# Optimization experiments

Measured on AMD Instinct MI355X. Metric: run time of the kernel, lower is better.

Reference implementation:

```python
import jax, jax.numpy as jnp
import numpy as np
import math

K = 30   # neighbors
T = 9    # num_kernel

def sparsemax(z):
    # sparsemax along last axis
    zs = jnp.sort(z, axis=-1)[..., ::-1]
    rng = jnp.arange(1, z.shape[-1] + 1, dtype=z.dtype)
    cs = jnp.cumsum(zs, axis=-1)
    support = (1.0 + rng * zs) > cs
    kz = jnp.sum(support, axis=-1, keepdims=True)
    tau = (jnp.take_along_axis(cs, kz - 1, axis=-1) - 1.0) / kz.astype(z.dtype)
    return jnp.maximum(z - tau, 0.0)

def bn(x, g, b, axes, eps=1e-5):
    # batch-norm (training-mode batch stats), channel axis = 1
    m = jnp.mean(x, axes, keepdims=True)
    v = jnp.var(x, axes, keepdims=True)
    sh = [1] * x.ndim; sh[1] = -1
    return (x - m) / jnp.sqrt(v + eps) * g.reshape(sh) + b.reshape(sh)

def _forward(x, B_ff, mlp_W, permx, W1, b1, S1, W2, b2, S2, W3, b3, S3, W4, b4, S4,
             W5, g5, be5, L1, g6, be6, L2, bL2, g7, be7, L3, bL3):
    Bsz, _, N = x.shape
    pts = jnp.transpose(x, (0, 2, 1))                      # [B,N,3]
    # knn (DGCNN-style): negative squared distance, top-k (self first)
    xx = jnp.sum(pts * pts, -1)                            # [B,N]
    inner = jnp.einsum('bnc,bmc->bnm', pts, pts)
    negd = 2.0 * inner - xx[:, :, None] - xx[:, None, :]
    _, idx = jax.lax.top_k(negd, K)                        # [B,N,K] int32
    gather = jax.vmap(lambda f, i: f[i])                   # [B,N,F],[B,N,K]->[B,N,K,F]
    # Fourier features -> sparsemax basis weights -> per-point permatrix
    ng = gather(pts, idx)                                  # [B,N,K,3]
    xrep = jnp.broadcast_to(ng[:, :, :1, :], ng.shape)     # self repeated
    rel = ng - xrep
    sq = jnp.sum(rel * rel, -1, keepdims=True)
    dist = jnp.where(sq > 0, jnp.sqrt(jnp.where(sq > 0, sq, 1.0)), 0.0)  # safe norm
    feats = jnp.concatenate([xrep, rel, dist], -1).reshape(Bsz, N, 7 * K)
    ff = (2.0 * math.pi) * (feats @ B_ff)                  # [B,N,32]
    ff = jnp.concatenate([jnp.sin(ff), jnp.cos(ff)], -1)   # [B,N,64]
    w = sparsemax(ff @ mlp_W)                              # [B,N,16]
    P = jnp.einsum('bni,ikt->bnkt', w, permx)              # [B,N,K,T]

    def paiconv(f, W, b, S):  # f: [B,Cin,N]
        ft = jnp.transpose(f, (0, 2, 1))                   # [B,N,Cin]
        nb = gather(ft, idx)                               # [B,N,K,Cin]
        agg = jnp.einsum('bnkc,bnkt->bntc', nb, P).reshape(Bsz, N, -1)
        out = agg @ W + b + ft @ S                         # [B,N,Cout]
        return jnp.transpose(out, (0, 2, 1))

    gelu = lambda a: jax.nn.gelu(a, approximate=False)
    x1 = gelu(paiconv(x,  W1, b1, S1))
    x2 = gelu(paiconv(x1, W2, b2, S2))
    x3 = gelu(paiconv(x2, W3, b3, S3))
    x4 = gelu(paiconv(x3, W4, b4, S4))
    f = jnp.concatenate([x1, x2, x3, x4], 1)               # [B,512,N]
    f = jnp.einsum('bcn,ce->ben', f, W5)                   # conv5 (1x1)
    f = gelu(bn(f, g5, be5, (0, 2)))
    h = jnp.concatenate([jnp.max(f, -1), jnp.mean(f, -1)], -1)  # [B,2048]
    h = gelu(bn(h @ L1, g6, be6, (0,)))
    h = gelu(bn(h @ L2 + bL2, g7, be7, (0,)))
    return h @ L3 + bL3


def setup_inputs() -> dict:
    key = jax.random.key(0)
    ks = jax.random.split(key, 20)
    rn = lambda k_, sh, s=1.0: jax.random.normal(k_, sh, dtype=jnp.float32) * s
    B, N = 16, 1024
    inp = {}
    inp['x'] = rn(ks[0], (B, 3, N))
    inp['B_ff'] = rn(ks[1], (7 * K, 32))
    inp['mlp_W'] = rn(ks[2], (64, 16), 0.125)
    inp['permx'] = rn(ks[3], (16, K, T), 0.1)
    dims = [(3, 64), (64, 64), (64, 128), (128, 256)]
    for i, (ci, co) in enumerate(dims, 1):
        inp['W%d' % i] = rn(ks[3 + i], (T * ci, co), 1.0 / float(np.sqrt(T * ci)))
        inp['b%d' % i] = jnp.zeros((co,), jnp.float32)
        inp['S%d' % i] = rn(ks[7 + i], (ci, co), 1.0 / float(np.sqrt(ci)))
    inp['W5'] = rn(ks[12], (512, 1024), 1.0 / float(np.sqrt(512)))
    inp['g5'] = jnp.ones((1024,), jnp.float32); inp['be5'] = jnp.zeros((1024,), jnp.float32)
    inp['L1'] = rn(ks[13], (2048, 512), 1.0 / float(np.sqrt(2048)))
    inp['g6'] = jnp.ones((512,), jnp.float32); inp['be6'] = jnp.zeros((512,), jnp.float32)
    inp['L2'] = rn(ks[14], (512, 256), 1.0 / float(np.sqrt(512))); inp['bL2'] = jnp.zeros((256,), jnp.float32)
    inp['g7'] = jnp.ones((256,), jnp.float32); inp['be7'] = jnp.zeros((256,), jnp.float32)
    inp['L3'] = rn(ks[15], (256, 40), 1.0 / float(np.sqrt(256))); inp['bL3'] = jnp.zeros((40,), jnp.float32)
    return inp


def reference(x, B_ff, mlp_W, permx, W1, b1, S1, W2, b2, S2, W3, b3, S3, W4, b4, S4,
              W5, g5, be5, L1, g6, be6, L2, bL2, g7, be7, L3, bL3):
    return _forward(x, B_ff, mlp_W, permx, W1, b1, S1, W2, b2, S2, W3, b3, S3, W4, b4, S4,
                    W5, g5, be5, L1, g6, be6, L2, bL2, g7, be7, L3, bL3)
```

## Files before the change

kernel.cpp:

```cpp
#include <hip/hip_runtime.h>
#include <hip/hip_bf16.h>
#include <cstddef>

#define BSZ 16
#define NPT 1024
#define KNN 30
#define TKR 9
#define FLT_BIG 3.402823466e+38f

typedef unsigned short u16;
typedef __attribute__((ext_vector_type(8))) u16 u16x8;
typedef __attribute__((ext_vector_type(4))) float f32x4;

__device__ __forceinline__ float gelu_f(float x) {
    return 0.5f * x * (1.0f + erff(x * 0.7071067811865476f));
}

__device__ __forceinline__ u16 bf16_rne(float a) {
    unsigned u = __float_as_uint(a);
    u += 0x7FFFu + ((u >> 16) & 1u);
    return (u16)(u >> 16);
}
__device__ __forceinline__ float bf16_tof(u16 h) {
    return __uint_as_float(((unsigned)h) << 16);
}
__device__ __forceinline__ void split_bf16(float a, u16& h, u16& l) {
    h = bf16_rne(a);
    float r = a - bf16_tof(h);
    l = bf16_rne(r);
}

__device__ __forceinline__ size_t pack_off(int row, int k, int npanels_row) {
    return (size_t)((k >> 5) * npanels_row + (row >> 7)) * 4096
         + (size_t)(((k >> 3) & 3) * 1024 + (row & 127) * 8 + (k & 7));
}

__global__ __launch_bounds__(256) void prep_all(
    const float* __restrict__ x, float* __restrict__ pts,
    const float* __restrict__ W1, const float* __restrict__ S1, float* __restrict__ wz1,
    const float* __restrict__ W2, const float* __restrict__ S2, float* __restrict__ wz2,
    const float* __restrict__ W3, const float* __restrict__ S3, float* __restrict__ wz3,
    const float* __restrict__ W4, const float* __restrict__ S4,
    u16* __restrict__ w4tH, u16* __restrict__ w4tL) {
    int layer = blockIdx.y;
    int t = blockIdx.x * 256 + threadIdx.x;
    if (layer == 0) {
        if (t >= BSZ * NPT) return;
        int b = t >> 10, n = t & 1023;
        const float* xp = x + (size_t)b * 3 * NPT;
        pts[t * 3 + 0] = xp[n];
        pts[t * 3 + 1] = xp[NPT + n];
        pts[t * 3 + 2] = xp[2 * NPT + n];
        return;
    }
    if (layer == 4) {
        if (t >= 1280 * 256) return;
        int k = t >> 8, n = t & 255;
        float v = (k < 1152) ? W4[(size_t)k * 256 + n] : S4[(size_t)(k - 1152) * 256 + n];
        u16 h, l;
        split_bf16(v, h, l);
        size_t off = pack_off(n, k, 2);
        w4tH[off] = h;
        w4tL[off] = l;
        return;
    }
    const float *W, *S; float* WZ; int KW, KS, N, kpad;
    if (layer == 1)      { W = W1; S = S1; WZ = wz1; KW = 27;   KS = 3;   N = 64;  kpad = 32;  }
    else if (layer == 2) { W = W2; S = S2; WZ = wz2; KW = 576;  KS = 64;  N = 64;  kpad = 640; }
    else                 { W = W3; S = S3; WZ = wz3; KW = 576;  KS = 64;  N = 128; kpad = 640; }
    if (t >= kpad * N) return;
    int k = t / N, n = t - k * N;
    float v = 0.0f;
    if (k < KW) v = W[(size_t)k * N + n];
    else if (k < KW + KS) v = S[(size_t)(k - KW) * N + n];
    WZ[t] = v;
}

__global__ __launch_bounds__(256) void knn_basis_kernel(
    const float* __restrict__ pts, const float* __restrict__ B_ff,
    const float* __restrict__ mlp_W, const float* __restrict__ permx,
    int* __restrict__ idx, float* __restrict__ P) {
    __shared__ float npt[4][KNN * 3];
    __shared__ float feats[4][7 * KNN];
    __shared__ float sc[4][64];
    __shared__ float zl[4][16];
    __shared__ float w[4][16];
    __shared__ float sZs[4][16];
    __shared__ float sCs[4][16];
    __shared__ int sIds[4][KNN];
    int tid = threadIdx.x;
    int wave = tid >> 6, lane = tid & 63;
    int bn_ = blockIdx.x * 4 + wave;
    int b = bn_ >> 10;

    {
        double px = (double)pts[(size_t)bn_ * 3 + 0];
        double py = (double)pts[(size_t)bn_ * 3 + 1];
        double pz = (double)pts[(size_t)bn_ * 3 + 2];
        double xn = px * px + py * py + pz * pz;
        const float* pb = pts + (size_t)(b << 10) * 3;
        int base = lane * 16;
        unsigned mono[16];
        #pragma unroll
        for (int j = 0; j < 16; j++) {
            int m = base + j;
            double qx = (double)pb[m * 3 + 0];
            double qy = (double)pb[m * 3 + 1];
            double qz = (double)pb[m * 3 + 2];
            double inner = px * qx + py * qy + pz * qz;
            double xm = qx * qx + qy * qy + qz * qz;
            double cd = 2.0 * inner - xn - xm;
            float cf = (float)cd;
            unsigned bb = __float_as_uint(cf);
            mono[j] = (bb & 0x80000000u) ? ~bb : (bb | 0x80000000u);
        }
        unsigned alive = 0xFFFFu;
        unsigned c1v = 0u, c2v = 0u;
        int c1j = 0, c2j = 0;
        #pragma unroll
        for (int j = 0; j < 16; j++) {
            unsigned v = mono[j];
            if (v > c1v) { c2v = c1v; c2j = c1j; c1v = v; c1j = j; }
            else if (v > c2v) { c2v = v; c2j = j; }
        }
        bool have2 = true;
        for (int it = 0; it < KNN; it++) {
            unsigned m = c1v;
            #pragma unroll
            for (int s = 1; s < 64; s <<= 1) {
                unsigned ov = (unsigned)__shfl_xor((int)m, s, 64);
                m = (ov > m) ? ov : m;
            }
            unsigned long long ball = __ballot(c1v == m);
            int wlan = (int)__builtin_ctzll(ball);
            int jw = __shfl(c1j, wlan, 64);
            int bi = (wlan << 4) + jw;
            if (lane == it) sIds[wave][it] = bi;
            if (lane == wlan) {
                alive &= ~(1u << c1j);
                if (have2) {
                    c1v = c2v; c1j = c2j; have2 = false;
                } else {
                    unsigned a1 = 0u, a2 = 0u;
                    int j1 = 0, j2 = 0;
                    #pragma unroll
                    for (int j = 0; j < 16; j++) {
                        unsigned v = ((alive >> j) & 1u) ? mono[j] : 0u;
                        if (v > a1) { a2 = a1; j2 = j1; a1 = v; j1 = j; }
                        else if (v > a2) { a2 = v; j2 = j; }
                    }
                    c1v = a1; c1j = j1; c2v = a2; c2j = j2;
                    have2 = true;
                }
            }
        }
        __builtin_amdgcn_wave_barrier();
        if (lane < KNN) idx[(size_t)bn_ * KNN + lane] = sIds[wave][lane];
    }
    __syncthreads();

    if (lane < KNN) {
        int m = sIds[wave][lane];
        const float* q = pts + ((size_t)(b << 10) + m) * 3;
        npt[wave][lane * 3 + 0] = q[0];
        npt[wave][lane * 3 + 1] = q[1];
        npt[wave][lane * 3 + 2] = q[2];
    }
    __syncthreads();
    if (lane < KNN) {
        float sx = npt[wave][0], sy = npt[wave][1], sz = npt[wave][2];
        float rx = npt[wave][lane * 3 + 0] - sx;
        float ry = npt[wave][lane * 3 + 1] - sy;
        float rz = npt[wave][lane * 3 + 2] - sz;
        float sq = rx * rx + ry * ry + rz * rz;
        float dist = (sq > 0.0f) ? sqrtf(sq) : 0.0f;
        feats[wave][lane * 7 + 0] = sx;
        feats[wave][lane * 7 + 1] = sy;
        feats[wave][lane * 7 + 2] = sz;
        feats[wave][lane * 7 + 3] = rx;
        feats[wave][lane * 7 + 4] = ry;
        feats[wave][lane * 7 + 5] = rz;
        feats[wave][lane * 7 + 6] = dist;
    }
    __syncthreads();
    {
        int j = lane & 31;
        int half = lane >> 5;
        int i0 = half * 105;
        float acc = 0.0f;
        for (int i = i0; i < i0 + 105; i++) acc += feats[wave][i] * B_ff[i * 32 + j];
        acc += __shfl_xor(acc, 32, 64);
        if (half == 0) {
            float ffv = 6.283185307179586f * acc;
            sc[wave][j] = sinf(ffv);
            sc[wave][j + 32] = cosf(ffv);
        }
    }
    __syncthreads();
    {
        int j = lane & 15;
        int h = lane >> 4;
        float acc = 0.0f;
        for (int i = 16 * h; i < 16 * h + 16; i++) acc += sc[wave][i] * mlp_W[i * 16 + j];
        acc += __shfl_xor(acc, 16, 64);
        acc += __shfl_xor(acc, 32, 64);
        if (h == 0) zl[wave][j] = acc;
    }
    __syncthreads();
    {
        int l = lane & 15;
        float zv = zl[wave][l];
        int rank = 0;
        #pragma unroll
        for (int j = 0; j < 16; j++) {
            float zj = zl[wave][j];
            rank += (zj > zv || (zj == zv && j < l)) ? 1 : 0;
        }
        if (lane < 16) sZs[wave][rank] = zv;
        __builtin_amdgcn_wave_barrier();
        float cs = 0.0f;
        #pragma unroll
        for (int p = 0; p < 16; p++) {
            float zp = sZs[wave][p];
            cs += (p <= l) ? zp : 0.0f;
        }
        float zsl = sZs[wave][l];
        bool flag = (lane < 16) && (1.0f + (float)(l + 1) * zsl > cs);
        unsigned long long ball = __ballot(flag);
        int cnt = (int)__popcll(ball & 0xFFFFull);
        if (lane < 16) sCs[wave][l] = cs;
        __builtin_amdgcn_wave_barrier();
        float tau = (sCs[wave][cnt - 1] - 1.0f) / (float)cnt;
        if (lane < 16) w[wave][l] = fmaxf(zv - tau, 0.0f);
    }
    __syncthreads();
    float* Pp = P + (size_t)bn_ * (KNN * TKR);
    for (int e = lane; e < KNN * TKR; e += 64) {
        int k = e / TKR, t = e - TKR * k;
        float acc = 0.0f;
        for (int i = 0; i < 16; i++) acc += w[wave][i] * permx[(i * KNN + k) * TKR + t];
        Pp[e] = acc;
    }
}

template <int CIN>
__global__ __launch_bounds__(256) void agg_kernel(
    const float* __restrict__ ft, int ftst,
    const float* __restrict__ P, const int* __restrict__ idx,
    float* __restrict__ Z, int kpad) {
    __shared__ float sP[KNN * TKR];
    __shared__ float sNb[KNN * CIN];
    __shared__ int sIdx[KNN];
    int bn_ = blockIdx.x;
    int b = bn_ >> 10;
    int tid = threadIdx.x;
    if (tid < KNN) sIdx[tid] = idx[(size_t)bn_ * KNN + tid];
    for (int e = tid; e < KNN * TKR; e += 256) sP[e] = P[(size_t)bn_ * (KNN * TKR) + e];
    __syncthreads();
    for (int e = tid; e < KNN * CIN; e += 256) {
        int k = e / CIN, c = e - k * CIN;
        sNb[e] = ft[((size_t)(b << 10) + sIdx[k]) * ftst + c];
    }
    __syncthreads();
    float* zp = Z + (size_t)bn_ * kpad;
    const int KW = TKR * CIN;
    for (int e = tid; e < kpad; e += 256) {
        float v;
        if (e < KW) {
            int t = e / CIN, c = e - t * CIN;
            float acc = 0.0f;
            #pragma unroll
            for (int k = 0; k < KNN; k++) acc += sNb[k * CIN + c] * sP[k * TKR + t];
            v = acc;
        } else if (e < KW + CIN) {
            v = ft[(size_t)bn_ * ftst + (e - KW)];
        } else {
            v = 0.0f;
        }
        zp[e] = v;
    }
}

template <int CIN>
__global__ __launch_bounds__(256) void agg_v_kernel(
    const float* __restrict__ ft, int ftst,
    const float* __restrict__ P, const int* __restrict__ idx,
    float* __restrict__ Z, int kpad) {
    __shared__ float sP[KNN * TKR];
    __shared__ float sNb[KNN * CIN];
    __shared__ int sIdx[KNN];
    constexpr int C4 = CIN / 4;
    int bn_ = blockIdx.x;
    int b = bn_ >> 10;
    int tid = threadIdx.x;
    if (tid < KNN) sIdx[tid] = idx[(size_t)bn_ * KNN + tid];
    for (int e = tid; e < KNN * TKR; e += 256) sP[e] = P[(size_t)bn_ * (KNN * TKR) + e];
    __syncthreads();
    for (int e = tid; e < KNN * C4; e += 256) {
        int k = e / C4, c4 = (e - k * C4) * 4;
        *(float4*)&sNb[k * CIN + c4] =
            *(const float4*)&ft[((size_t)(b << 10) + sIdx[k]) * ftst + c4];
    }
    __syncthreads();
    float* zp = Z + (size_t)bn_ * kpad;
    const int KW = TKR * CIN;
    for (int e = tid; e < (kpad >> 2); e += 256) {
        int c0 = e * 4;
        float4 v;
        if (c0 < KW) {
            int t = c0 / CIN, c4 = c0 - t * CIN;
            float4 a = make_float4(0.f, 0.f, 0.f, 0.f);
            #pragma unroll
            for (int k = 0; k < KNN; k++) {
                float p = sP[k * TKR + t];
                float4 nb = *(const float4*)&sNb[k * CIN + c4];
                a.x += nb.x * p; a.y += nb.y * p;
                a.z += nb.z * p; a.w += nb.w * p;
            }
            v = a;
        } else if (c0 < KW + CIN) {
            v = *(const float4*)&ft[(size_t)bn_ * ftst + (c0 - KW)];
        } else {
            v = make_float4(0.f, 0.f, 0.f, 0.f);
        }
        *(float4*)&zp[c0] = v;
    }
}

__global__ __launch_bounds__(256) void agg_v_split4_kernel(
    const float* __restrict__ ft, int ftst,
    const float* __restrict__ P, const int* __restrict__ idx,
    u16* __restrict__ ZH, u16* __restrict__ ZL) {
    __shared__ int   sIdx4[4][KNN];
    __shared__ float sP4[4][KNN * TKR + 2];
    __shared__ float sNb4[4][KNN * 128];
    __shared__ __align__(16) u16 oH[4][640];
    __shared__ __align__(16) u16 oL[4][640];
    int tid = threadIdx.x;
    int wave = tid >> 6, lane = tid & 63;
    int r0 = blockIdx.x << 2;
    int b = r0 >> 10;
    const int KW = TKR * 128;

    if (tid < 4 * KNN) {
        int row = tid / KNN, k = tid - row * KNN;
        sIdx4[row][k] = idx[(size_t)(r0 + row) * KNN + k];
    }
    for (int e = tid; e < 4 * KNN * TKR; e += 256) {
        int row = e / (KNN * TKR), i = e - row * (KNN * TKR);
        sP4[row][i] = P[(size_t)(r0 + row) * (KNN * TKR) + i];
    }
    __syncthreads();
    for (int e = tid; e < 4 * KNN * 32; e += 256) {
        int row = e / (KNN * 32), rem = e - row * (KNN * 32);
        int k = rem >> 5, c4 = (rem & 31) << 2;
        *(float4*)&sNb4[row][k * 128 + c4] =
            *(const float4*)&ft[((size_t)(b << 10) + sIdx4[row][k]) * ftst + c4];
    }
    __syncthreads();

    #pragma unroll
    for (int pass = 0; pass < 2; pass++) {
        int ebase = pass * 640;
        for (int q = lane; q < 160; q += 64) {
            int e0 = ebase + q * 4;
            float4 v;
            if (e0 < KW) {
                int t = e0 >> 7, c = e0 & 127;
                float4 a = make_float4(0.f, 0.f, 0.f, 0.f);
                #pragma unroll
                for (int k = 0; k < KNN; k++) {
                    float p = sP4[wave][k * TKR + t];
                    float4 nb = *(const float4*)&sNb4[wave][k * 128 + c];
                    a.x += nb.x * p; a.y += nb.y * p;
                    a.z += nb.z * p; a.w += nb.w * p;
                }
                v = a;
            } else if (e0 < KW + 128) {
                v = *(const float4*)&ft[(size_t)(r0 + wave) * ftst + (e0 - KW)];
            } else {
                v = make_float4(0.f, 0.f, 0.f, 0.f);
            }
            u16 h[4], l[4];
            split_bf16(v.x, h[0], l[0]);
            split_bf16(v.y, h[1], l[1]);
            split_bf16(v.z, h[2], l[2]);
            split_bf16(v.w, h[3], l[3]);
            uint2 hv, lv;
            hv.x = (unsigned)h[0] | ((unsigned)h[1] << 16);
            hv.y = (unsigned)h[2] | ((unsigned)h[3] << 16);
            lv.x = (unsigned)l[0] | ((unsigned)l[1] << 16);
            lv.y = (unsigned)l[2] | ((unsigned)l[3] << 16);
            *(uint2*)&oH[wave][q * 4] = hv;
            *(uint2*)&oL[wave][q * 4] = lv;
        }
        __syncthreads();
        for (int u = tid; u < 640; u += 256) {
            int kpl = u >> 5, s = u & 31;
            int kc = s >> 3, row = (s >> 1) & 3, half = s & 1;
            int eloc = kpl * 32 + kc * 8 + half * 4;
            uint2 hv = *(const uint2*)&oH[row][eloc];
            uint2 lv = *(const uint2*)&oL[row][eloc];
            size_t off = (size_t)((pass * 20 + kpl) * 128 + (r0 >> 7)) * 4096
                       + (size_t)(kc * 1024 + ((r0 & 127) + row) * 8 + half * 4);
            *(uint2*)&ZH[off] = hv;
            *(uint2*)&ZL[off] = lv;
        }
        __syncthreads();
    }
}

template <bool GELU, bool HASBIAS>
__global__ __launch_bounds__(256) void gemm_f32_64db(
    const float* __restrict__ A, int lda,
    const float* __restrict__ B, int ldb, int K,
    const float* __restrict__ bias,
    float* __restrict__ C, int ldc) {
    __shared__ float As[2][16][64];
    __shared__ float Bs[2][16][64];
    int tid = threadIdx.x;
    int tx = tid & 15, ty = tid >> 4;
    int m0 = blockIdx.y * 64, n0 = blockIdx.x * 64;
    float acc[4][4];
    #pragma unroll
    for (int i = 0; i < 4; i++)
        #pragma unroll
        for (int j = 0; j < 4; j++) acc[i][j] = 0.0f;

    int ar = tid >> 2, ac0 = (tid & 3) * 4;
    const float* aptr = A + (size_t)(m0 + ar) * lda + ac0;
    int br = tid >> 4, bc = (tid & 15) * 4;
    const float* bptr = B + (size_t)br * ldb + n0 + bc;

    float4 pa = *(const float4*)(aptr);
    float4 pb = *(const float4*)(bptr);
    As[0][ac0 + 0][ar] = pa.x; As[0][ac0 + 1][ar] = pa.y;
    As[0][ac0 + 2][ar] = pa.z; As[0][ac0 + 3][ar] = pa.w;
    *(float4*)&Bs[0][br][bc] = pb;
    __syncthreads();

    int nk = K >> 4;
    for (int t = 0; t < nk; t++) {
        int buf = t & 1;
        bool more = (t + 1) < nk;
        if (more) {
            int k0 = (t + 1) << 4;
            pa = *(const float4*)(aptr + k0);
            pb = *(const float4*)(bptr + (size_t)k0 * ldb);
        }
        #pragma unroll
        for (int kk = 0; kk < 16; kk++) {
            float av[4], bv[4];
            *(float4*)&av[0] = *(const float4*)&As[buf][kk][ty * 4];
            *(float4*)&bv[0] = *(const float4*)&Bs[buf][kk][tx * 4];
            #pragma unroll
            for (int i = 0; i < 4; i++)
                #pragma unroll
                for (int j = 0; j < 4; j++) acc[i][j] += av[i] * bv[j];
        }
        if (more) {
            int nb = 1 - buf;
            As[nb][ac0 + 0][ar] = pa.x; As[nb][ac0 + 1][ar] = pa.y;
            As[nb][ac0 + 2][ar] = pa.z; As[nb][ac0 + 3][ar] = pa.w;
            *(float4*)&Bs[nb][br][bc] = pb;
        }
        __syncthreads();
    }
    #pragma unroll
    for (int i = 0; i < 4; i++) {
        int r = m0 + ty * 4 + i;
        int c = n0 + tx * 4;
        float v[4];
        #pragma unroll
        for (int j = 0; j < 4; j++) {
            float t = acc[i][j];
            if (HASBIAS) t += bias[c + j];
            if (GELU) t = gelu_f(t);
            v[j] = t;
        }
        *(float4*)(C + (size_t)r * ldc + c) = *(float4*)v;
    }
}

__global__ __launch_bounds__(256) void convert_split(
    const float* __restrict__ feat, u16* __restrict__ fH, u16* __restrict__ fL,
    const float* __restrict__ W5, u16* __restrict__ wH, u16* __restrict__ wL) {
    int t = blockIdx.x * 256 + threadIdx.x;
    if (blockIdx.y == 0) {
        int T = t >> 9, s = t & 511;
        int kc = s >> 7, rloc = s & 127;
        int kp = T >> 7, rp = T & 127;
        int row = (rp << 7) + rloc;
        int k0 = (kp << 5) + (kc << 3);
        const float* fp = &feat[(size_t)row * 512 + k0];
        float4 a = *(const float4*)fp;
        float4 b = *(const float4*)(fp + 4);
        float v[8] = {a.x, a.y, a.z, a.w, b.x, b.y, b.z, b.w};
        u16 h[8], l[8];
        #pragma unroll
        for (int i = 0; i < 8; i++) split_bf16(v[i], h[i], l[i]);
        uint4 hv, lv;
        hv.x = (unsigned)h[0] | ((unsigned)h[1] << 16);
        hv.y = (unsigned)h[2] | ((unsigned)h[3] << 16);
        hv.z = (unsigned)h[4] | ((unsigned)h[5] << 16);
        hv.w = (unsigned)h[6] | ((unsigned)h[7] << 16);
        lv.x = (unsigned)l[0] | ((unsigned)l[1] << 16);
        lv.y = (unsigned)l[2] | ((unsigned)l[3] << 16);
        lv.z = (unsigned)l[4] | ((unsigned)l[5] << 16);
        lv.w = (unsigned)l[6] | ((unsigned)l[7] << 16);
        size_t off = (size_t)T * 4096 + kc * 1024 + rloc * 8;
        *(uint4*)&fH[off] = hv;
        *(uint4*)&fL[off] = lv;
    } else {
        if (t >= 512 * 1024) return;
        int n = t >> 9, k = t & 511;
        u16 h, l;
        split_bf16(W5[(size_t)k * 1024 + n], h, l);
        size_t off = pack_off(n, k, 8);
        wH[off] = h; wL[off] = l;
    }
}

template <bool STATS, bool GELU, bool HASBIAS>
__global__ __launch_bounds__(256) void mfma_bf16x3(
    const u16* __restrict__ fH, const u16* __restrict__ fL,
    const u16* __restrict__ wH, const u16* __restrict__ wL,
    int K, const float* __restrict__ bias,
    float* __restrict__ C, int ldc,
    float* __restrict__ partS, float* __restrict__ partQ) {
    __shared__ __align__(16) u16 lds[2][16384];
    int tid = threadIdx.x;
    int lane = tid & 63, wave = tid >> 6;
    int wr = wave >> 1, wc = wave & 1;
    int kg = lane >> 4, r = lane & 15;

    int nwg = gridDim.x * gridDim.y;
    int hw = blockIdx.y * gridDim.x + blockIdx.x;
    int logical = (hw & 7) * (nwg >> 3) + (hw >> 3);
    int nb = logical % gridDim.x;
    int mb = logical / gridDim.x;
    int m0 = mb << 7, n0 = nb << 7;
    int nmp = gridDim.y;
    int nnp = gridDim.x;

    const u16* src = (wave == 0) ? fH : (wave == 1) ? fL
                   : (wave == 2) ? wH : wL;

    f32x4 acc[4][4];
    #pragma unroll
    for (int i = 0; i < 4; i++)
        #pragma unroll
        for (int j = 0; j < 4; j++) {
            acc[i][j][0] = 0.0f; acc[i][j][1] = 0.0f;
            acc[i][j][2] = 0.0f; acc[i][j][3] = 0.0f;
        }

#define STAGE_K(BUF, TT) {                                                     \
    size_t tb = ((size_t)((wave < 2) ? ((TT) * nmp + mb)                       \
                                     : ((TT) * nnp + nb)) << 12);              \
    _Pragma("unroll")                                                          \
    for (int iw = 0; iw < 8; iw++) {                                           \
        const u16* gp = src + tb + (size_t)(((iw << 6) + lane) << 3);          \
        __builtin_amdgcn_global_load_lds(                                      \
            (const __attribute__((address_space(1))) void*)gp,                 \
            (__attribute__((address_space(3))) void*)&lds[BUF][(wave << 12) + (iw << 9)], \
            16, 0, 0);                                                         \
    } }

    int nk = K >> 5;
    STAGE_K(0, 0);
    __syncthreads();
    for (int t = 0; t < nk; t++) {
        if (t + 1 < nk) STAGE_K((t + 1) & 1, (t + 1));
        const u16* lb = lds[t & 1];
        u16x8 bh[4], bl[4];
        #pragma unroll
        for (int fj = 0; fj < 4; fj++) {
            int bcol = (wc << 6) + (fj << 4) + r;
            bh[fj] = *(const u16x8*)&lb[ 8192 + (((kg << 7) + bcol) << 3)];
            bl[fj] = *(const u16x8*)&lb[12288 + (((kg << 7) + bcol) << 3)];
        }
        #pragma unroll
        for (int fi = 0; fi < 4; fi++) {
            int arow = (wr << 6) + (fi << 4) + r;
            u16x8 ah = *(const u16x8*)&lb[       (((kg << 7) + arow) << 3)];
            u16x8 al = *(const u16x8*)&lb[4096 + (((kg << 7) + arow) << 3)];
            #pragma unroll
            for (int fj = 0; fj < 4; fj++) {
                asm volatile("v_mfma_f32_16x16x32_bf16 %0, %1, %2, %0"
                             : "+v"(acc[fi][fj]) : "v"(ah), "v"(bh[fj]));
                asm volatile("v_mfma_f32_16x16x32_bf16 %0, %1, %2, %0"
                             : "+v"(acc[fi][fj]) : "v"(ah), "v"(bl[fj]));
                asm volatile("v_mfma_f32_16x16x32_bf16 %0, %1, %2, %0"
                             : "+v"(acc[fi][fj]) : "v"(al), "v"(bh[fj]));
            }
        }
        __syncthreads();
    }
#undef STAGE_K

    asm volatile("s_nop 15\n\ts_nop 15" ::: "memory");

    float bvv[4];
    if (HASBIAS) {
        #pragma unroll
        for (int fj = 0; fj < 4; fj++) bvv[fj] = bias[n0 + (wc << 6) + (fj << 4) + r];
    }

    #pragma unroll
    for (int fi = 0; fi < 4; fi++)
        #pragma unroll
        for (int ri = 0; ri < 4; ri++) {
            int row = m0 + (wr << 6) + (fi << 4) + (kg << 2) + ri;
            float* cp = C + (size_t)row * ldc + n0 + (wc << 6) + r;
            #pragma unroll
            for (int fj = 0; fj < 4; fj++) {
                float v = acc[fi][fj][ri];
                if (HASBIAS) v += bvv[fj];
                if (GELU) v = gelu_f(v);
                cp[fj << 4] = v;
            }
        }

    if (STATS) {
        __syncthreads();
        float* sS = (float*)lds;
        float* sQ = sS + 1024;
        int slot = (wr << 2) + kg;
        #pragma unroll
        for (int fj = 0; fj < 4; fj++) {
            float s = 0.0f, q = 0.0f;
            #pragma unroll
            for (int fi = 0; fi < 4; fi++)
                #pragma unroll
                for (int ri = 0; ri < 4; ri++) {
                    float v = acc[fi][fj][ri];
                    s += v; q += v * v;
                }
            int cl = (wc << 6) + (fj << 4) + r;
            sS[slot * 128 + cl] = s;
            sQ[slot * 128 + cl] = q;
        }
        __syncthreads();
        if (tid < 128) {
            float S = 0.0f, Q = 0.0f;
            #pragma unroll
            for (int i = 0; i < 8; i++) { S += sS[i * 128 + tid]; Q += sQ[i * 128 + tid]; }
            partS[(size_t)mb * 1024 + n0 + tid] = S;
            partQ[(size_t)mb * 1024 + n0 + tid] = Q;
        }
    }
}

__global__ __launch_bounds__(256) void stats_reduce(
    const float* __restrict__ partS, const float* __restrict__ partQ,
    const float* __restrict__ g, const float* __restrict__ be,
    float* __restrict__ scaleb, float* __restrict__ shiftb) {
    int e = blockIdx.x * 256 + threadIdx.x;
    if (e >= 1024) return;
    double s = 0.0, q = 0.0;
    for (int mb = 0; mb < 128; mb++) {
        s += (double)partS[(size_t)mb * 1024 + e];
        q += (double)partQ[(size_t)mb * 1024 + e];
    }
    double m = s * (1.0 / 16384.0);
    double v = q * (1.0 / 16384.0) - m * m;
    float sc = g[e] * (float)(1.0 / sqrt(v + 1e-5));
    scaleb[e] = sc;
    shiftb[e] = be[e] - (float)m * sc;
}

__global__ __launch_bounds__(256) void pool_partial(
    const float* __restrict__ f5, const float* __restrict__ scaleb,
    const float* __restrict__ shiftb,
    float* __restrict__ partM, double* __restrict__ partSd) {
    int chunk = blockIdx.x, g = blockIdx.y, b = blockIdx.z;
    int tid = threadIdx.x;
    int lane = tid & 63, nlane = tid >> 6;
    int c0 = (g << 8) + lane * 4;
    float4 sc = *(const float4*)&scaleb[c0];
    float4 sh = *(const float4*)&shiftb[c0];
    float m0 = -FLT_BIG, m1 = -FLT_BIG, m2 = -FLT_BIG, m3 = -FLT_BIG;
    double s0 = 0.0, s1 = 0.0, s2 = 0.0, s3 = 0.0;
    int nend = (chunk + 1) << 6;
    for (int n = (chunk << 6) + nlane; n < nend; n += 4) {
        float4 v = *(const float4*)&f5[((size_t)(b << 10) + n) * 1024 + c0];
        float g0 = gelu_f(v.x * sc.x + sh.x);
        float g1 = gelu_f(v.y * sc.y + sh.y);
        float g2 = gelu_f(v.z * sc.z + sh.z);
        float g3 = gelu_f(v.w * sc.w + sh.w);
        m0 = fmaxf(m0, g0); m1 = fmaxf(m1, g1);
        m2 = fmaxf(m2, g2); m3 = fmaxf(m3, g3);
        s0 += (double)g0; s1 += (double)g1;
        s2 += (double)g2; s3 += (double)g3;
    }
    __shared__ float smax[4][256];
    __shared__ double ssum[4][256];
    *(float4*)&smax[nlane][lane * 4] = make_float4(m0, m1, m2, m3);
    ssum[nlane][lane * 4 + 0] = s0;
    ssum[nlane][lane * 4 + 1] = s1;
    ssum[nlane][lane * 4 + 2] = s2;
    ssum[nlane][lane * 4 + 3] = s3;
    __syncthreads();
    if (nlane == 0) {
        size_t base = ((size_t)((b * 4 + g) * 16 + chunk)) * 256 + lane * 4;
        #pragma unroll
        for (int j = 0; j < 4; j++) {
            float mm = smax[0][lane * 4 + j];
            double ss = ssum[0][lane * 4 + j];
            #pragma unroll
            for (int i = 1; i < 4; i++) {
                mm = fmaxf(mm, smax[i][lane * 4 + j]);
                ss += ssum[i][lane * 4 + j];
            }
            partM[base + j] = mm;
            partSd[base + j] = ss;
        }
    }
}

__global__ __launch_bounds__(256) void pool_finish(
    const float* __restrict__ partM, const double* __restrict__ partSd,
    float* __restrict__ h) {
    int b = blockIdx.x;
    int e0 = threadIdx.x * 4;
    int g = e0 >> 8, cl = e0 & 255;
    float mm[4] = {-FLT_BIG, -FLT_BIG, -FLT_BIG, -FLT_BIG};
    double ss[4] = {0.0, 0.0, 0.0, 0.0};
    for (int chunk = 0; chunk < 16; chunk++) {
        size_t base = ((size_t)((b * 4 + g) * 16 + chunk)) * 256 + cl;
        float4 pm = *(const float4*)&partM[base];
        mm[0] = fmaxf(mm[0], pm.x); mm[1] = fmaxf(mm[1], pm.y);
        mm[2] = fmaxf(mm[2], pm.z); mm[3] = fmaxf(mm[3], pm.w);
        ss[0] += partSd[base + 0]; ss[1] += partSd[base + 1];
        ss[2] += partSd[base + 2]; ss[3] += partSd[base + 3];
    }
    #pragma unroll
    for (int j = 0; j < 4; j++) {
        h[(size_t)b * 2048 + e0 + j] = mm[j];
        h[(size_t)b * 2048 + 1024 + e0 + j] = (float)(ss[j] * (1.0 / 1024.0));
    }
}

__global__ __launch_bounds__(256) void fc_split(
    const float* __restrict__ X, const float* __restrict__ W,
    double* __restrict__ part, int Bn, int In, int Out, int KC) {
    int tid = blockIdx.x * 256 + threadIdx.x;
    if (tid >= Bn * Out * KC) return;
    int chunk = tid / (Bn * Out);
    int r = tid - chunk * (Bn * Out);
    int b = r / Out, j = r - b * Out;
    int len = In / KC;
    int i0 = chunk * len;
    const float* x = X + (size_t)b * In + i0;
    const float* w = W + (size_t)i0 * Out + j;
    double acc = 0.0;
    for (int i = 0; i < len; i++) acc += (double)x[i] * (double)w[(size_t)i * Out];
    part[tid] = acc;
}

__global__ __launch_bounds__(256) void fc_bn_gelu(
    const double* __restrict__ part, const float* __restrict__ bias,
    const float* __restrict__ g, const float* __restrict__ be,
    float* __restrict__ Y, int Out, int KC) {
    int j = blockIdx.x * 256 + threadIdx.x;
    if (j >= Out) return;
    float r[BSZ];
    for (int b = 0; b < BSZ; b++) {
        double acc = bias ? (double)bias[j] : 0.0;
        for (int c = 0; c < KC; c++) acc += part[(size_t)c * (BSZ * Out) + b * Out + j];
        r[b] = (float)acc;
    }
    double m = 0.0;
    for (int b = 0; b < BSZ; b++) m += (double)r[b];
    m /= (double)BSZ;
    double v = 0.0;
    for (int b = 0; b < BSZ; b++) {
        double dd = (double)r[b] - m;
        v += dd * dd;
    }
    v /= (double)BSZ;
    float sc = g[j] * (float)(1.0 / sqrt(v + 1e-5));
    float sh = be[j] - (float)m * sc;
    for (int b = 0; b < BSZ; b++) Y[b * Out + j] = gelu_f(r[b] * sc + sh);
}

__global__ __launch_bounds__(256) void fc_reduce(
    const double* __restrict__ part, const float* __restrict__ bias,
    float* __restrict__ Y, int Bn, int Out, int KC) {
    int r = blockIdx.x * 256 + threadIdx.x;
    if (r >= Bn * Out) return;
    int j = r % Out;
    double acc = bias ? (double)bias[j] : 0.0;
    for (int c = 0; c < KC; c++) acc += part[(size_t)c * (Bn * Out) + r];
    Y[r] = (float)acc;
}

extern "C" void kernel_launch(void* const* d_in, const int* in_sizes, int n_in,
                              void* d_out, int out_size, void* d_ws, size_t ws_size,
                              hipStream_t stream) {
    const float* x     = (const float*)d_in[0];
    const float* B_ff  = (const float*)d_in[1];
    const float* mlp_W = (const float*)d_in[2];
    const float* permx = (const float*)d_in[3];
    const float* W1 = (const float*)d_in[4];
    const float* b1 = (const float*)d_in[5];
    const float* S1 = (const float*)d_in[6];
    const float* W2 = (const float*)d_in[7];
    const float* b2 = (const float*)d_in[8];
    const float* S2 = (const float*)d_in[9];
    const float* W3 = (const float*)d_in[10];
    const float* b3 = (const float*)d_in[11];
    const float* S3 = (const float*)d_in[12];
    const float* W4 = (const float*)d_in[13];
    const float* b4 = (const float*)d_in[14];
    const float* S4 = (const float*)d_in[15];
    const float* W5 = (const float*)d_in[16];
    const float* g5 = (const float*)d_in[17];
    const float* be5 = (const float*)d_in[18];
    const float* L1 = (const float*)d_in[19];
    const float* g6 = (const float*)d_in[20];
    const float* be6 = (const float*)d_in[21];
    const float* L2 = (const float*)d_in[22];
    const float* bL2 = (const float*)d_in[23];
    const float* g7 = (const float*)d_in[24];
    const float* be7 = (const float*)d_in[25];
    const float* L3 = (const float*)d_in[26];
    const float* bL3 = (const float*)d_in[27];
    float* outp = (float*)d_out;

    const int BN = BSZ * NPT;

    float* ws = (float*)d_ws;
    float* pts   = ws;
    int*   idxb  = (int*)(ws + 49152);
    float* Pb    = ws + 540672;
    float* feat  = Pb + 4423680;
    float* Zbig  = feat + 8388608;
    u16*   ZH    = (u16*)Zbig;
    u16*   ZL    = (u16*)(Zbig + 10485760);
    float* f5    = Zbig;
    u16*   featH = (u16*)(Zbig + 16777216);
    float* poolM = Zbig + 16777216;
    double* poolS = (double*)(Zbig + 16777216 + 262144);
    float* w4slot = Zbig + 20971520;
    u16*   w4tH  = (u16*)w4slot;
    u16*   w4tL  = w4tH + 327680;
    float* scb   = w4slot + 327680;
    float* shb   = scb + 1024;
    float* hb    = shb + 1024;
    float* y1    = hb + 32768;
    float* y2    = y1 + 8192;
    float* partC_S = y2 + 4096;
    float* partC_Q = partC_S + 131072;
    double* partF  = (double*)(partC_Q + 131072);
    float* wsend = (float*)(partF + 131072);
    u16* featL = (u16*)ws;
    u16* w5tH  = (u16*)(ws + 4194304);
    u16* w5tL  = (u16*)(ws + 4456448);
    float* wz1   = Zbig + 11010048;
    float* wz2   = wz1 + 2048;
    float* wz3   = wz2 + 40960;
    size_t need_bytes = (size_t)(wsend - ws) * sizeof(float);
    if (ws_size < need_bytes) return;

    prep_all<<<dim3(1280, 5), 256, 0, stream>>>(
        x, pts, W1, S1, wz1, W2, S2, wz2, W3, S3, wz3, W4, S4, w4tH, w4tL);

    knn_basis_kernel<<<BN / 4, 256, 0, stream>>>(pts, B_ff, mlp_W, permx, idxb, Pb);

    agg_kernel<3><<<BN, 256, 0, stream>>>(pts, 3, Pb, idxb, Zbig, 32);
    gemm_f32_64db<true, true><<<dim3(1, 256), 256, 0, stream>>>(
        Zbig, 32, wz1, 64, 32, b1, feat + 0, 512);
    agg_v_kernel<64><<<BN, 256, 0, stream>>>(feat + 0, 512, Pb, idxb, Zbig, 640);
    gemm_f32_64db<true, true><<<dim3(1, 256), 256, 0, stream>>>(
        Zbig, 640, wz2, 64, 640, b2, feat + 64, 512);
    agg_v_kernel<64><<<BN, 256, 0, stream>>>(feat + 64, 512, Pb, idxb, Zbig, 640);
    gemm_f32_64db<true, true><<<dim3(2, 256), 256, 0, stream>>>(
        Zbig, 640, wz3, 128, 640, b3, feat + 128, 512);
    agg_v_split4_kernel<<<BN / 4, 256, 0, stream>>>(feat + 128, 512, Pb, idxb, ZH, ZL);
    mfma_bf16x3<false, true, true><<<dim3(2, 128), 256, 0, stream>>>(
        ZH, ZL, w4tH, w4tL, 1280, b4, feat + 256, 512, nullptr, nullptr);

    convert_split<<<dim3(4096, 2), 256, 0, stream>>>(feat, featH, featL, W5, w5tH, w5tL);
    mfma_bf16x3<true, false, false><<<dim3(8, 128), 256, 0, stream>>>(
        featH, featL, w5tH, w5tL, 512, nullptr, f5, 1024, partC_S, partC_Q);

    stats_reduce<<<4, 256, 0, stream>>>(partC_S, partC_Q, g5, be5, scb, shb);
    pool_partial<<<dim3(16, 4, BSZ), 256, 0, stream>>>(f5, scb, shb, poolM, poolS);
    pool_finish<<<BSZ, 256, 0, stream>>>(poolM, poolS, hb);

    fc_split<<<(BSZ * 512 * 16 + 255) / 256, 256, 0, stream>>>(hb, L1, partF, BSZ, 2048, 512, 16);
    fc_bn_gelu<<<2, 256, 0, stream>>>(partF, nullptr, g6, be6, y1, 512, 16);
    fc_split<<<(BSZ * 256 * 8 + 255) / 256, 256, 0, stream>>>(y1, L2, partF, BSZ, 512, 256, 8);
    fc_bn_gelu<<<1, 256, 0, stream>>>(partF, bL2, g7, be7, y2, 256, 8);
    fc_split<<<(BSZ * 40 * 4 + 255) / 256, 256, 0, stream>>>(y2, L3, partF, BSZ, 256, 40, 4);
    fc_reduce<<<(BSZ * 40 + 255) / 256, 256, 0, stream>>>(partF, bL3, outp, BSZ, 40, 4);
}
```

Measured before the change: 788.7 us.

## Restructure layer-4 aggregation to 8 rows per block with register accumulators

The layer-4 aggregation kernel now handles 8 points per block, with 32 threads per point each owning 4 channels. Each thread keeps all 9 kernel-tap accumulators in registers and reads neighbor features straight from global memory, with no shared-memory neighbor staging. The two-pass output transpose becomes a single pass over a wider shared buffer, which cuts the block syncs and makes each global store cover 8 contiguous rows per kc chunk. In exchange it uses more registers per thread, and the neighbor loads are uncached gathers.

```diff
diff --git a/kernel.cpp b/kernel.cpp
--- a/kernel.cpp
+++ b/kernel.cpp
@@ -327,86 +327,77 @@
     }
 }
 
-__global__ __launch_bounds__(256) void agg_v_split4_kernel(
+__global__ __launch_bounds__(256) void agg_v_split8_kernel(
     const float* __restrict__ ft, int ftst,
     const float* __restrict__ P, const int* __restrict__ idx,
     u16* __restrict__ ZH, u16* __restrict__ ZL) {
-    __shared__ int   sIdx4[4][KNN];
-    __shared__ float sP4[4][KNN * TKR + 2];
-    __shared__ float sNb4[4][KNN * 128];
-    __shared__ __align__(16) u16 oH[4][640];
-    __shared__ __align__(16) u16 oL[4][640];
+    __shared__ int   sIdx8[8][KNN];
+    __shared__ float sP8[8][KNN * TKR];
+    __shared__ __align__(16) u16 oH[8][1288];
+    __shared__ __align__(16) u16 oL[8][1288];
     int tid = threadIdx.x;
-    int wave = tid >> 6, lane = tid & 63;
-    int r0 = blockIdx.x << 2;
+    int row = tid >> 5;
+    int cq = tid & 31;
+    int c0 = cq << 2;
+    int r0 = blockIdx.x << 3;
     int b = r0 >> 10;
-    const int KW = TKR * 128;
-
-    if (tid < 4 * KNN) {
-        int row = tid / KNN, k = tid - row * KNN;
-        sIdx4[row][k] = idx[(size_t)(r0 + row) * KNN + k];
-    }
-    for (int e = tid; e < 4 * KNN * TKR; e += 256) {
-        int row = e / (KNN * TKR), i = e - row * (KNN * TKR);
-        sP4[row][i] = P[(size_t)(r0 + row) * (KNN * TKR) + i];
-    }
-    __syncthreads();
-    for (int e = tid; e < 4 * KNN * 32; e += 256) {
-        int row = e / (KNN * 32), rem = e - row * (KNN * 32);
-        int k = rem >> 5, c4 = (rem & 31) << 2;
-        *(float4*)&sNb4[row][k * 128 + c4] =
-            *(const float4*)&ft[((size_t)(b << 10) + sIdx4[row][k]) * ftst + c4];
-    }
-    __syncthreads();
-
+
+    if (tid < 8 * KNN) {
+        int r = tid / KNN, k = tid - r * KNN;
+        sIdx8[r][k] = idx[(size_t)(r0 + r) * KNN + k];
+    }
+    for (int e = tid; e < 8 * KNN * TKR; e += 256) {
+        int r = e / (KNN * TKR), i = e - r * (KNN * TKR);
+        sP8[r][i] = P[(size_t)(r0 + r) * (KNN * TKR) + i];
+    }
+    __syncthreads();
+
+    float4 acc[9];
     #pragma unroll
-    for (int pass = 0; pass < 2; pass++) {
-        int ebase = pass * 640;
-        for (int q = lane; q < 160; q += 64) {
-            int e0 = ebase + q * 4;
-            float4 v;
-            if (e0 < KW) {
-                int t = e0 >> 7, c = e0 & 127;
-                float4 a = make_float4(0.f, 0.f, 0.f, 0.f);
-                #pragma unroll
-                for (int k = 0; k < KNN; k++) {
-                    float p = sP4[wave][k * TKR + t];
-                    float4 nb = *(const float4*)&sNb4[wave][k * 128 + c];
-                    a.x += nb.x * p; a.y += nb.y * p;
-                    a.z += nb.z * p; a.w += nb.w * p;
-                }
-                v = a;
-            } else if (e0 < KW + 128) {
-                v = *(const float4*)&ft[(size_t)(r0 + wave) * ftst + (e0 - KW)];
-            } else {
-                v = make_float4(0.f, 0.f, 0.f, 0.f);
-            }
-            u16 h[4], l[4];
-            split_bf16(v.x, h[0], l[0]);
-            split_bf16(v.y, h[1], l[1]);
-            split_bf16(v.z, h[2], l[2]);
-            split_bf16(v.w, h[3], l[3]);
-            uint2 hv, lv;
-            hv.x = (unsigned)h[0] | ((unsigned)h[1] << 16);
-            hv.y = (unsigned)h[2] | ((unsigned)h[3] << 16);
-            lv.x = (unsigned)l[0] | ((unsigned)l[1] << 16);
-            lv.y = (unsigned)l[2] | ((unsigned)l[3] << 16);
-            *(uint2*)&oH[wave][q * 4] = hv;
-            *(uint2*)&oL[wave][q * 4] = lv;
-        }
-        __syncthreads();
-        for (int u = tid; u < 640; u += 256) {
-            int kpl = u >> 5, s = u & 31;
-            int kc = s >> 3, row = (s >> 1) & 3, half = s & 1;
-            int eloc = kpl * 32 + kc * 8 + half * 4;
-            uint2 hv = *(const uint2*)&oH[row][eloc];
-            uint2 lv = *(const uint2*)&oL[row][eloc];
-            size_t off = (size_t)((pass * 20 + kpl) * 128 + (r0 >> 7)) * 4096
-                       + (size_t)(kc * 1024 + ((r0 & 127) + row) * 8 + half * 4);
-            *(uint2*)&ZH[off] = hv;
-            *(uint2*)&ZL[off] = lv;
-        }
-        __syncthreads();
+    for (int t = 0; t < 9; t++) acc[t] = make_float4(0.f, 0.f, 0.f, 0.f);
+    const float* fb = ft + (size_t)(b << 10) * ftst;
+    for (int k = 0; k < KNN; k++) {
+        float4 nb = *(const float4*)&fb[(size_t)sIdx8[row][k] * ftst + c0];
+        #pragma unroll
+        for (int t = 0; t < 9; t++) {
+            float p = sP8[row][k * TKR + t];
+            acc[t].x += nb.x * p; acc[t].y += nb.y * p;
+            acc[t].z += nb.z * p; acc[t].w += nb.w * p;
+        }
+    }
+    float4 self = *(const float4*)&ft[(size_t)(r0 + row) * ftst + c0];
+
+    #pragma unroll
+    for (int t = 0; t < 10; t++) {
+        float4 v = (t < 9) ? acc[t] : self;
+        int e0 = (t < 9) ? (t * 128 + c0) : (1152 + c0);
+        u16 h[4], l[4];
+        split_bf16(v.x, h[0], l[0]);
+        split_bf16(v.y, h[1], l[1]);
+        split_bf16(v.z, h[2], l[2]);
+        split_bf16(v.w, h[3], l[3]);
+        uint2 hv, lv;
+        hv.x = (unsigned)h[0] | ((unsigned)h[1] << 16);
+        hv.y = (unsigned)h[2] | ((unsigned)h[3] << 16);
+        lv.x = (unsigned)l[0] | ((unsigned)l[1] << 16);
+        lv.y = (unsigned)l[2] | ((unsigned)l[3] << 16);
+        *(uint2*)&oH[row][e0] = hv;
+        *(uint2*)&oL[row][e0] = lv;
+    }
+    __syncthreads();
+
+    for (int u = tid; u < 2560; u += 256) {
+        int kp = u >> 6;
+        int l = u & 63;
+        int kc = l >> 4, rg = (l >> 3) & 1, rw = (l >> 1) & 3, half = l & 1;
+        int rloc = rg * 4 + rw;
+        int eloc = kp * 32 + kc * 8 + half * 4;
+        uint2 hv = *(const uint2*)&oH[rloc][eloc];
+        uint2 lv = *(const uint2*)&oL[rloc][eloc];
+        size_t off = (size_t)(kp * 128 + (r0 >> 7)) * 4096
+                   + (size_t)(kc * 1024 + ((r0 & 127) + rloc) * 8 + half * 4);
+        *(uint2*)&ZH[off] = hv;
+        *(uint2*)&ZL[off] = lv;
     }
 }
 
@@ -878,7 +869,7 @@
     agg_v_kernel<64><<<BN, 256, 0, stream>>>(feat + 64, 512, Pb, idxb, Zbig, 640);
     gemm_f32_64db<true, true><<<dim3(2, 256), 256, 0, stream>>>(
         Zbig, 640, wz3, 128, 640, b3, feat + 128, 512);
-    agg_v_split4_kernel<<<BN / 4, 256, 0, stream>>>(feat + 128, 512, Pb, idxb, ZH, ZL);
+    agg_v_split8_kernel<<<BN / 8, 256, 0, stream>>>(feat + 128, 512, Pb, idxb, ZH, ZL);
     mfma_bf16x3<false, true, true><<<dim3(2, 128), 256, 0, stream>>>(
         ZH, ZL, w4tH, w4tL, 1280, b4, feat + 256, 512, nullptr, nullptr);
 
```

After: 690.6 us. 1.14x faster.
